# Optimization experiments

Measured on AMD Instinct MI355X. Metric: run time of the kernel, lower is better.

The kernel has to match this reference:

```python
import jax, jax.numpy as jnp
import numpy as np

B, N, F_IN = 4, 2048, 256
K, D = 4, 64
NEG_SLOPE = 0.2


def setup_inputs() -> dict:
    key = jax.random.key(0)
    k1, k2, k3, k4, k5 = jax.random.split(key, 5)
    x = jax.random.normal(k1, (B, N, F_IN), dtype=jnp.float32)
    adj = jax.random.randint(k2, (B, N, N), 0, 2, dtype=jnp.int32)
    # xavier_uniform-style params
    def xavier(k, shape):
        fan_in, fan_out = shape[-2], shape[-1]
        lim = np.sqrt(6.0 / (fan_in + fan_out))
        return jax.random.uniform(k, shape, jnp.float32, -lim, lim)
    W = xavier(k3, (K, F_IN, D))
    a_src = xavier(k4, (K, D, 1))
    a_dst = xavier(k5, (K, D, 1))
    return {"x": x, "adj": adj, "W": W, "a_src": a_src, "a_dst": a_dst}


def reference(x, adj, W, a_src, a_dst):
    # Wh: (B, K, N, D)
    Wh = jnp.einsum('bnf,kfd->bknd', x, W)
    e_src = jnp.einsum('bknd,kdo->bkno', Wh, a_src)  # (B,K,N,1)
    e_dst = jnp.einsum('bknd,kdo->bkno', Wh, a_dst)  # (B,K,N,1)
    e = e_src + jnp.swapaxes(e_dst, -2, -1)          # (B,K,N,N)
    e = jnp.where(e > 0, e, NEG_SLOPE * e)           # LeakyReLU(0.2)
    # adjacency mask with forced self-loops (adj + I > 0)
    eye = jnp.eye(e.shape[-1], dtype=bool)
    mask = (adj[:, None, :, :] > 0) | eye            # (B,1|K,N,N)
    e = jnp.where(mask, e, -jnp.inf)
    # numerically-stable softmax matching F_module_softmax
    x_max = jnp.max(e, axis=-1, keepdims=True)
    x_max = jnp.where(jnp.isinf(x_max), 0.0, x_max)
    exp_e = jnp.exp(e - x_max)
    exp_e = jnp.where(jnp.isinf(e), 0.0, exp_e)
    alpha = exp_e / (jnp.sum(exp_e, axis=-1, keepdims=True) + 1e-10)
    # dropout is identity in eval mode
    out = jnp.matmul(alpha, Wh)                      # (B,K,N,D)
    # concat heads: (B,N,K*D)
    Bn, Kn, Nn, Dn = out.shape
    return jnp.transpose(out, (0, 2, 1, 3)).reshape(Bn, Nn, Kn * Dn)
```

## Files before the change

### kernel.cpp

```cpp
#include <hip/hip_runtime.h>

#define NB 4
#define NN 2048
#define NF 256
#define NK 4
#define ND 64
#define NEG 0.2f
#define LOG2E 1.4426950408889634f

typedef _Float16 f16;
typedef _Float16 f16x4 __attribute__((ext_vector_type(4)));
typedef _Float16 f16x8 __attribute__((ext_vector_type(8)));
typedef float f32x4 __attribute__((ext_vector_type(4)));

__device__ __forceinline__ int sz2(int d) { return ((d >> 1) ^ (d >> 3)) & 3; }

__global__ __launch_bounds__(256) void k01(
    const float* __restrict__ x,
    const int*   __restrict__ adj,
    const float* __restrict__ Wm,
    const float* __restrict__ a_src,
    const float* __restrict__ a_dst,
    unsigned int* __restrict__ abit,
    f16* __restrict__ wht,
    float* __restrict__ sbuf,
    float* __restrict__ ebuf,
    float* __restrict__ fbuf)
{
    __shared__ f16 wt[64 * 256];

    const int bx  = blockIdx.x;
    const int tid = threadIdx.x;

    if (bx >= 256) {
        const int row = (bx - 256) * 4 + (tid >> 6);
        const int l   = tid & 63;
        const int i   = row & (NN - 1);
        const int* __restrict__ ar = adj + (size_t)row * NN;

        int v[32];
#pragma unroll
        for (int c = 0; c < 32; ++c) v[c] = ar[c * 64 + l];

        unsigned int kx = 0, ky = 0;
#pragma unroll
        for (int c = 0; c < 32; ++c) {
            unsigned long long m = __ballot(v[c] > 0);
            if (l == c) { kx = (unsigned int)m; ky = (unsigned int)(m >> 32); }
        }
        if (l == (i >> 6)) {
            unsigned int sb = 1u << (i & 31);
            if (((i >> 5) & 1) == 0) kx |= sb; else ky |= sb;
        }
        if (l < 32) {
            uint2 kk; kk.x = kx; kk.y = ky;
            *(uint2*)&abit[(size_t)row * 64 + l * 2] = kk;
        }
        return;
    }

    const int gx  = bx & 15;
    const int k   = (bx >> 4) & 3;
    const int b   = bx >> 6;
    const int wv  = tid >> 6;
    const int l   = tid & 63;
    const int q   = l >> 4;
    const int r16 = l & 15;

    for (int fc = 0; fc < 64; ++fc) {
        int f = fc * 4 + wv;
        int d = l;
        wt[d * 256 + (f ^ ((d & 7) << 3))] = (f16)Wm[(k * NF + f) * ND + d];
    }
    __syncthreads();

    const int ncol0 = gx * 128 + wv * 32;
    f32x4 acc[2][4];
#pragma unroll
    for (int nt = 0; nt < 2; ++nt)
#pragma unroll
        for (int dt = 0; dt < 4; ++dt)
            acc[nt][dt] = (f32x4){0.f, 0.f, 0.f, 0.f};

    for (int fs = 0; fs < 16; ++fs) {
        const int f0 = fs * 16 + q * 4;
        f16x4 af[4];
#pragma unroll
        for (int dt = 0; dt < 4; ++dt) {
            int d = dt * 16 + r16;
            af[dt] = *(const f16x4*)&wt[d * 256 + (f0 ^ ((d & 7) << 3))];
        }
#pragma unroll
        for (int nt = 0; nt < 2; ++nt) {
            int n = ncol0 + nt * 16 + r16;
            float4 xv = *(const float4*)&x[((size_t)(b * NN + n)) * NF + f0];
            f16x4 bf = {(f16)xv.x, (f16)xv.y, (f16)xv.z, (f16)xv.w};
#pragma unroll
            for (int dt = 0; dt < 4; ++dt)
                acc[nt][dt] = __builtin_amdgcn_mfma_f32_16x16x16f16(
                    af[dt], bf, acc[nt][dt], 0, 0, 0);
        }
    }

    float asv[4][4], adv[4][4];
#pragma unroll
    for (int dt = 0; dt < 4; ++dt)
#pragma unroll
        for (int rr = 0; rr < 4; ++rr) {
            int d = dt * 16 + q * 4 + rr;
            asv[dt][rr] = a_src[k * ND + d];
            adv[dt][rr] = a_dst[k * ND + d];
        }

    const int jt = gx * 4 + wv;
    f16* __restrict__ tile = wht + ((size_t)(b * NK + k) * 64 + jt) * 2048;
    const int qj = r16 >> 2, ee = r16 & 3;

#pragma unroll
    for (int nt = 0; nt < 2; ++nt) {
        int n = ncol0 + nt * 16 + r16;
        float sp = 0.f, tp = 0.f;
#pragma unroll
        for (int dt = 0; dt < 4; ++dt)
#pragma unroll
            for (int rr = 0; rr < 4; ++rr) {
                float v = acc[nt][dt][rr];
                int d = dt * 16 + q * 4 + rr;
                tile[d * 32 + ((qj ^ sz2(d)) << 3) + nt * 4 + ee] = (f16)v;
                sp += v * asv[dt][rr];
                tp += v * adv[dt][rr];
            }
        sp += __shfl_xor(sp, 16);
        sp += __shfl_xor(sp, 32);
        tp += __shfl_xor(tp, 16);
        tp += __shfl_xor(tp, 32);
        if (q == 0) {
            int idx = (b * NK + k) * NN + n;
            sbuf[idx] = sp;
            ebuf[idx] = __builtin_exp2f(tp * LOG2E);
            fbuf[idx] = __builtin_exp2f(0.2f * LOG2E * tp);
        }
    }
}

__global__ __launch_bounds__(512, 4) void k2_attn(
    const unsigned int* __restrict__ abit,
    const f16* __restrict__ wht,
    const float* __restrict__ sbuf,
    const float* __restrict__ ebuf,
    const float* __restrict__ fbuf,
    float* __restrict__ out)
{
    const int i0  = blockIdx.x * 64;
    const int k   = blockIdx.y;
    const int b   = blockIdx.z;
    const int tid = threadIdx.x;
    const int w   = tid >> 6;
    const int c   = w >> 2;
    const int rw  = w & 3;
    const int l   = tid & 63;
    const int q   = l >> 4;
    const int r16 = l & 15;
    const int iglob = i0 + rw * 16 + r16;

    __shared__ char pool[66048];
    float* el   = (float*)(pool + 49152);
    float* fl   = (float*)(pool + 57344);
    float* dden = (float*)(pool + 65536);

    const unsigned int* __restrict__ abrow =
        abit + (size_t)(b * NN + iglob) * 64 + c * 32;
    uint2 abx[16];
#pragma unroll
    for (int it = 0; it < 16; ++it) abx[it] = *(const uint2*)(abrow + it * 2);

    {
        const float* eb = ebuf + (b * NK + k) * NN;
        const float* fb = fbuf + (b * NK + k) * NN;
        *(float4*)&el[tid * 4] = *(const float4*)&eb[tid * 4];
        *(float4*)&fl[tid * 4] = *(const float4*)&fb[tid * 4];
    }

    const float s  = sbuf[(b * NK + k) * NN + iglob];
    const float Af = __builtin_exp2f(0.8f * LOG2E * fminf(s, 0.f));
    const float Bf = __builtin_exp2f(-0.8f * LOG2E * fmaxf(s, 0.f));
    const char* gtiles = (const char*)(wht + (size_t)(b * NK + k) * 64 * 2048);

    float denom = 0.f;
    f32x4 acc[4];
#pragma unroll
    for (int dt = 0; dt < 4; ++dt) acc[dt] = (f32x4){0.f, 0.f, 0.f, 0.f};

#define STAGE8(bb, it)                                                         \
    do {                                                                       \
        const char* gsrc = gtiles + (size_t)(c * 1024 + (it) * 64) * 128 +     \
                           (tid & 255) * 16;                                   \
        char* ldst = pool + c * 24576 + (bb) * 8192 + (w & 3) * 1024;          \
        __builtin_amdgcn_global_load_lds(                                      \
            (const __attribute__((address_space(1))) void*)gsrc,               \
            (__attribute__((address_space(3))) void*)ldst, 16, 0, 0);          \
        __builtin_amdgcn_global_load_lds(                                      \
            (const __attribute__((address_space(1))) void*)(gsrc + 4096),      \
            (__attribute__((address_space(3))) void*)(ldst + 4096), 16, 0, 0); \
    } while (0)

    STAGE8(0, 0);
    STAGE8(1, 1);

#pragma unroll
    for (int it = 0; it < 16; ++it) {
        if (it < 15)
            asm volatile("s_waitcnt vmcnt(2) lgkmcnt(0)" ::: "memory");
        else
            asm volatile("s_waitcnt vmcnt(0) lgkmcnt(0)" ::: "memory");
        __builtin_amdgcn_sched_barrier(0);
        __builtin_amdgcn_s_barrier();
        __builtin_amdgcn_sched_barrier(0);
        if (it < 14) STAGE8((it + 2) % 3, it + 2);

        const char* lb0 = pool + c * 24576 + (it % 3) * 8192;
        const uint2 ab = abx[it];
#pragma unroll
        for (int h = 0; h < 2; ++h) {
            const unsigned int bits = h ? ab.y : ab.x;
            const unsigned int bs = bits >> (q * 4);
            const int tb = c * 1024 + it * 64 + h * 32;
            float4 e0 = *(const float4*)&el[tb + q * 4];
            float4 e1 = *(const float4*)&el[tb + 16 + q * 4];
            float4 f0 = *(const float4*)&fl[tb + q * 4];
            float4 f1 = *(const float4*)&fl[tb + 16 + q * 4];
            float ea[4] = {e0.x, e0.y, e0.z, e0.w};
            float eb[4] = {e1.x, e1.y, e1.z, e1.w};
            float fa[4] = {f0.x, f0.y, f0.z, f0.w};
            float fb[4] = {f1.x, f1.y, f1.z, f1.w};
            float w0[4], w1[4];
#pragma unroll
            for (int e = 0; e < 4; ++e) {
                float wa = fmaxf(Af * ea[e], Bf * fa[e]);
                w0[e] = (bs & (1u << e)) ? wa : 0.f;
                float wb = fmaxf(Af * eb[e], Bf * fb[e]);
                w1[e] = (bs & (1u << (16 + e))) ? wb : 0.f;
            }
            denom += ((w0[0] + w0[1]) + (w0[2] + w0[3])) +
                     ((w1[0] + w1[1]) + (w1[2] + w1[3]));
            f16x8 pa = {(f16)w0[0], (f16)w0[1], (f16)w0[2], (f16)w0[3],
                        (f16)w1[0], (f16)w1[1], (f16)w1[2], (f16)w1[3]};
            const char* lb = lb0 + h * 4096;
#pragma unroll
            for (int dt = 0; dt < 4; ++dt) {
                int d = dt * 16 + r16;
                f16x8 v8 = *(const f16x8*)(lb + d * 64 + ((q ^ sz2(d)) << 4));
                acc[dt] = __builtin_amdgcn_mfma_f32_16x16x32_f16(
                    pa, v8, acc[dt], 0, 0, 0);
            }
        }
    }
#undef STAGE8

    denom += __shfl_xor(denom, 16);
    denom += __shfl_xor(denom, 32);

    __syncthreads();
    float* stash = (float*)pool;
    if (c == 1) {
#pragma unroll
        for (int dt = 0; dt < 4; ++dt)
            *(f32x4*)&stash[(rw * 4 + dt) * 256 + l * 4] = acc[dt];
    }
    if (l < 16) dden[c * 64 + rw * 16 + l] = denom;
    __syncthreads();

    if (c == 0) {
#pragma unroll
        for (int dt = 0; dt < 4; ++dt)
            acc[dt] += *(const f32x4*)&stash[(rw * 4 + dt) * 256 + l * 4];
#pragma unroll
        for (int rr = 0; rr < 4; ++rr) {
            int irow = q * 4 + rr;
            float dd = dden[rw * 16 + irow] + dden[64 + rw * 16 + irow];
            float inv = 1.f / (dd + 1e-10f);
#pragma unroll
            for (int dt = 0; dt < 4; ++dt)
                out[((size_t)(b * NN) + i0 + rw * 16 + irow) * (NK * ND) +
                    k * ND + dt * 16 + r16] = acc[dt][rr] * inv;
        }
    }
}

extern "C" void kernel_launch(void* const* d_in, const int* in_sizes, int n_in,
                              void* d_out, int out_size, void* d_ws, size_t ws_size,
                              hipStream_t stream) {
    const float* x     = (const float*)d_in[0];
    const int*   adj   = (const int*)d_in[1];
    const float* Wm    = (const float*)d_in[2];
    const float* a_src = (const float*)d_in[3];
    const float* a_dst = (const float*)d_in[4];
    float* out = (float*)d_out;

    char* ws = (char*)d_ws;
    f16*   wht  = (f16*)ws;
    float* sbuf = (float*)(ws + (4u << 20));
    float* ebuf = (float*)(ws + (4u << 20) + (128u << 10));
    float* fbuf = (float*)(ws + (4u << 20) + (256u << 10));
    unsigned int* abit = (unsigned int*)(ws + (4u << 20) + (384u << 10));

    k01<<<dim3(256 + NB * NN / 4), 256, 0, stream>>>(
        x, adj, Wm, a_src, a_dst, abit, wht, sbuf, ebuf, fbuf);
    k2_attn<<<dim3(NN / 64, NK, NB), 512, 0, stream>>>(
        abit, wht, sbuf, ebuf, fbuf, out);
}
```

Before: 47.76 us.

## Switch attention kernel to 32x32 MFMA tiles with 128-row blocks and 4-way j split

The attention kernel now processes 128 query rows per block with 1024 threads, splitting the neighbor dimension four ways across wave groups and using 32x32x16 MFMA instead of 16x16x32. The Wh staging layout written by the first kernel is changed to 64-column slabs with an 8-way XOR swizzle to match the new LDS read pattern. The cross-group reduction stashes three partial accumulators with a swizzle and sums them in group 0. The aim is more reuse of each staged Wh tile across more rows and fewer MFMA issues. In exchange it needs much more LDS (about 114KB), which limits occupancy, and a heavier final reduction.

```diff
diff --git a/kernel.cpp b/kernel.cpp
--- a/kernel.cpp
+++ b/kernel.cpp
@@ -12,8 +12,9 @@
 typedef _Float16 f16x4 __attribute__((ext_vector_type(4)));
 typedef _Float16 f16x8 __attribute__((ext_vector_type(8)));
 typedef float f32x4 __attribute__((ext_vector_type(4)));
-
-__device__ __forceinline__ int sz2(int d) { return ((d >> 1) ^ (d >> 3)) & 3; }
+typedef float f32x16 __attribute__((ext_vector_type(16)));
+
+__device__ __forceinline__ int gsz(int d) { return (d ^ (d >> 3)) & 7; }
 
 __global__ __launch_bounds__(256) void k01(
     const float* __restrict__ x,
@@ -112,13 +113,12 @@
             adv[dt][rr] = a_dst[k * ND + d];
         }
 
-    const int jt = gx * 4 + wv;
-    f16* __restrict__ tile = wht + ((size_t)(b * NK + k) * 64 + jt) * 2048;
-    const int qj = r16 >> 2, ee = r16 & 3;
+    const size_t obase = (size_t)(b * NK + k) * 131072;
 
 #pragma unroll
     for (int nt = 0; nt < 2; ++nt) {
-        int n = ncol0 + nt * 16 + r16;
+        int n  = ncol0 + nt * 16 + r16;
+        int s_ = n >> 6, g = (n >> 3) & 7, e = n & 7;
         float sp = 0.f, tp = 0.f;
 #pragma unroll
         for (int dt = 0; dt < 4; ++dt)
@@ -126,7 +126,7 @@
             for (int rr = 0; rr < 4; ++rr) {
                 float v = acc[nt][dt][rr];
                 int d = dt * 16 + q * 4 + rr;
-                tile[d * 32 + ((qj ^ sz2(d)) << 3) + nt * 4 + ee] = (f16)v;
+                wht[obase + s_ * 4096 + d * 64 + ((g ^ gsz(d)) << 3) + e] = (f16)v;
                 sp += v * asv[dt][rr];
                 tp += v * adv[dt][rr];
             }
@@ -143,7 +143,7 @@
     }
 }
 
-__global__ __launch_bounds__(512, 4) void k2_attn(
+__global__ __launch_bounds__(1024, 4) void k2_attn(
     const unsigned int* __restrict__ abit,
     const f16* __restrict__ wht,
     const float* __restrict__ sbuf,
@@ -151,7 +151,7 @@
     const float* __restrict__ fbuf,
     float* __restrict__ out)
 {
-    const int i0  = blockIdx.x * 64;
+    const int i0  = blockIdx.x * 128;
     const int k   = blockIdx.y;
     const int b   = blockIdx.z;
     const int tid = threadIdx.x;
@@ -159,43 +159,46 @@
     const int c   = w >> 2;
     const int rw  = w & 3;
     const int l   = tid & 63;
-    const int q   = l >> 4;
-    const int r16 = l & 15;
-    const int iglob = i0 + rw * 16 + r16;
-
-    __shared__ char pool[66048];
-    float* el   = (float*)(pool + 49152);
-    float* fl   = (float*)(pool + 57344);
-    float* dden = (float*)(pool + 65536);
+    const int r32 = l & 31;
+    const int hi  = l >> 5;
+    const int iglob = i0 + rw * 32 + r32;
+
+    __shared__ __attribute__((aligned(16))) char pool[116736];
+    float* el   = (float*)(pool + 98304);
+    float* fl   = (float*)(pool + 106496);
+    float* dden = (float*)(pool + 114688);
 
     const unsigned int* __restrict__ abrow =
-        abit + (size_t)(b * NN + iglob) * 64 + c * 32;
-    uint2 abx[16];
-#pragma unroll
-    for (int it = 0; it < 16; ++it) abx[it] = *(const uint2*)(abrow + it * 2);
+        abit + (size_t)(b * NN + iglob) * 64 + c * 16;
+    uint2 abx[8];
+#pragma unroll
+    for (int it = 0; it < 8; ++it) abx[it] = *(const uint2*)(abrow + it * 2);
 
     {
         const float* eb = ebuf + (b * NK + k) * NN;
         const float* fb = fbuf + (b * NK + k) * NN;
-        *(float4*)&el[tid * 4] = *(const float4*)&eb[tid * 4];
-        *(float4*)&fl[tid * 4] = *(const float4*)&fb[tid * 4];
+        int t5 = tid & 511;
+        if (tid < 512) *(float4*)&el[t5 * 4] = *(const float4*)&eb[t5 * 4];
+        else           *(float4*)&fl[t5 * 4] = *(const float4*)&fb[t5 * 4];
     }
 
     const float s  = sbuf[(b * NK + k) * NN + iglob];
     const float Af = __builtin_exp2f(0.8f * LOG2E * fminf(s, 0.f));
     const float Bf = __builtin_exp2f(-0.8f * LOG2E * fmaxf(s, 0.f));
-    const char* gtiles = (const char*)(wht + (size_t)(b * NK + k) * 64 * 2048);
+    const char* gtiles = (const char*)wht + (size_t)(b * NK + k) * 262144;
 
     float denom = 0.f;
-    f32x4 acc[4];
-#pragma unroll
-    for (int dt = 0; dt < 4; ++dt) acc[dt] = (f32x4){0.f, 0.f, 0.f, 0.f};
+    f32x16 acc[2];
+#pragma unroll
+    for (int dh = 0; dh < 2; ++dh)
+#pragma unroll
+        for (int z = 0; z < 16; ++z) acc[dh][z] = 0.f;
 
 #define STAGE8(bb, it)                                                         \
     do {                                                                       \
-        const char* gsrc = gtiles + (size_t)(c * 1024 + (it) * 64) * 128 +     \
+        const char* gsrc = gtiles + (size_t)(c * 8 + (it)) * 8192 +            \
                            (tid & 255) * 16;                                   \
-        char* ldst = pool + c * 24576 + (bb) * 8192 + (w & 3) * 1024;          \
+        char* ldst = pool + c * 24576 + (bb) * 8192 + (tid & 255) * 16;        \
         __builtin_amdgcn_global_load_lds(                                      \
             (const __attribute__((address_space(1))) void*)gsrc,               \
             (__attribute__((address_space(3))) void*)ldst, 16, 0, 0);          \
@@ -204,85 +207,104 @@
             (__attribute__((address_space(3))) void*)(ldst + 4096), 16, 0, 0); \
     } while (0)
 
+    __builtin_amdgcn_sched_barrier(0);
     STAGE8(0, 0);
     STAGE8(1, 1);
 
 #pragma unroll
-    for (int it = 0; it < 16; ++it) {
-        if (it < 15)
-            asm volatile("s_waitcnt vmcnt(2) lgkmcnt(0)" ::: "memory");
-        else
-            asm volatile("s_waitcnt vmcnt(0) lgkmcnt(0)" ::: "memory");
+    for (int it = 0; it < 8; ++it) {
+        if (it < 7) asm volatile("s_waitcnt vmcnt(2) lgkmcnt(0)" ::: "memory");
+        else        asm volatile("s_waitcnt vmcnt(0) lgkmcnt(0)" ::: "memory");
         __builtin_amdgcn_sched_barrier(0);
         __builtin_amdgcn_s_barrier();
         __builtin_amdgcn_sched_barrier(0);
-        if (it < 14) STAGE8((it + 2) % 3, it + 2);
-
-        const char* lb0 = pool + c * 24576 + (it % 3) * 8192;
+        if (it < 6) STAGE8((it + 2) % 3, it + 2);
+
+        const char* lb = pool + c * 24576 + (it % 3) * 8192;
         const uint2 ab = abx[it];
 #pragma unroll
-        for (int h = 0; h < 2; ++h) {
-            const unsigned int bits = h ? ab.y : ab.x;
-            const unsigned int bs = bits >> (q * 4);
-            const int tb = c * 1024 + it * 64 + h * 32;
-            float4 e0 = *(const float4*)&el[tb + q * 4];
-            float4 e1 = *(const float4*)&el[tb + 16 + q * 4];
-            float4 f0 = *(const float4*)&fl[tb + q * 4];
-            float4 f1 = *(const float4*)&fl[tb + 16 + q * 4];
-            float ea[4] = {e0.x, e0.y, e0.z, e0.w};
-            float eb[4] = {e1.x, e1.y, e1.z, e1.w};
-            float fa[4] = {f0.x, f0.y, f0.z, f0.w};
-            float fb[4] = {f1.x, f1.y, f1.z, f1.w};
-            float w0[4], w1[4];
-#pragma unroll
-            for (int e = 0; e < 4; ++e) {
-                float wa = fmaxf(Af * ea[e], Bf * fa[e]);
-                w0[e] = (bs & (1u << e)) ? wa : 0.f;
-                float wb = fmaxf(Af * eb[e], Bf * fb[e]);
-                w1[e] = (bs & (1u << (16 + e))) ? wb : 0.f;
-            }
-            denom += ((w0[0] + w0[1]) + (w0[2] + w0[3])) +
-                     ((w1[0] + w1[1]) + (w1[2] + w1[3]));
-            f16x8 pa = {(f16)w0[0], (f16)w0[1], (f16)w0[2], (f16)w0[3],
-                        (f16)w1[0], (f16)w1[1], (f16)w1[2], (f16)w1[3]};
-            const char* lb = lb0 + h * 4096;
-#pragma unroll
-            for (int dt = 0; dt < 4; ++dt) {
-                int d = dt * 16 + r16;
-                f16x8 v8 = *(const f16x8*)(lb + d * 64 + ((q ^ sz2(d)) << 4));
-                acc[dt] = __builtin_amdgcn_mfma_f32_16x16x32_f16(
-                    pa, v8, acc[dt], 0, 0, 0);
+        for (int jj = 0; jj < 4; ++jj) {
+            const int jts = (jj + c) & 3;
+            const unsigned int word  = (jts & 2) ? ab.y : ab.x;
+            const unsigned int mbyte = (word >> (((jts & 1) << 4) + (hi << 3))) & 0xffu;
+            const int jb = c * 512 + it * 64 + jts * 16 + hi * 8;
+            float4 e0 = *(const float4*)&el[jb];
+            float4 e1 = *(const float4*)&el[jb + 4];
+            float4 f0 = *(const float4*)&fl[jb];
+            float4 f1 = *(const float4*)&fl[jb + 4];
+            float ev[8] = {e0.x, e0.y, e0.z, e0.w, e1.x, e1.y, e1.z, e1.w};
+            float fv[8] = {f0.x, f0.y, f0.z, f0.w, f1.x, f1.y, f1.z, f1.w};
+            float wv[8];
+#pragma unroll
+            for (int e = 0; e < 8; ++e) {
+                float m = fmaxf(Af * ev[e], Bf * fv[e]);
+                wv[e] = (mbyte & (1u << e)) ? m : 0.f;
+            }
+            denom += ((wv[0] + wv[1]) + (wv[2] + wv[3])) +
+                     ((wv[4] + wv[5]) + (wv[6] + wv[7]));
+            f16x8 pa = {(f16)wv[0], (f16)wv[1], (f16)wv[2], (f16)wv[3],
+                        (f16)wv[4], (f16)wv[5], (f16)wv[6], (f16)wv[7]};
+#pragma unroll
+            for (int dh = 0; dh < 2; ++dh) {
+                const int d = dh * 32 + r32;
+                f16x8 v8 = *(const f16x8*)(lb + d * 128 +
+                               ((((jts << 1) | hi) ^ gsz(d)) << 4));
+                acc[dh] = __builtin_amdgcn_mfma_f32_32x32x16_f16(
+                    pa, v8, acc[dh], 0, 0, 0);
             }
         }
     }
 #undef STAGE8
 
-    denom += __shfl_xor(denom, 16);
     denom += __shfl_xor(denom, 32);
 
     __syncthreads();
     float* stash = (float*)pool;
-    if (c == 1) {
-#pragma unroll
-        for (int dt = 0; dt < 4; ++dt)
-            *(f32x4*)&stash[(rw * 4 + dt) * 256 + l * 4] = acc[dt];
-    }
-    if (l < 16) dden[c * 64 + rw * 16 + l] = denom;
+    if (c != 0) {
+        float* sb = stash + ((c - 1) * 4 + rw) * 2048 + l * 16;
+#pragma unroll
+        for (int dh = 0; dh < 2; ++dh)
+#pragma unroll
+            for (int sub = 0; sub < 4; ++sub) {
+                f32x4 v = {acc[dh][sub * 4], acc[dh][sub * 4 + 1],
+                           acc[dh][sub * 4 + 2], acc[dh][sub * 4 + 3]};
+                *(f32x4*)&sb[dh * 1024 + ((sub ^ (l & 3)) << 2)] = v;
+            }
+    }
+    if (l < 32) dden[c * 128 + rw * 32 + l] = denom;
     __syncthreads();
 
     if (c == 0) {
 #pragma unroll
-        for (int dt = 0; dt < 4; ++dt)
-            acc[dt] += *(const f32x4*)&stash[(rw * 4 + dt) * 256 + l * 4];
-#pragma unroll
-        for (int rr = 0; rr < 4; ++rr) {
-            int irow = q * 4 + rr;
-            float dd = dden[rw * 16 + irow] + dden[64 + rw * 16 + irow];
-            float inv = 1.f / (dd + 1e-10f);
-#pragma unroll
-            for (int dt = 0; dt < 4; ++dt)
-                out[((size_t)(b * NN) + i0 + rw * 16 + irow) * (NK * ND) +
-                    k * ND + dt * 16 + r16] = acc[dt][rr] * inv;
+        for (int cc = 0; cc < 3; ++cc) {
+            const float* sr = stash + (cc * 4 + rw) * 2048 + l * 16;
+#pragma unroll
+            for (int dh = 0; dh < 2; ++dh)
+#pragma unroll
+                for (int sub = 0; sub < 4; ++sub) {
+                    f32x4 v = *(const f32x4*)&sr[dh * 1024 + ((sub ^ (l & 3)) << 2)];
+#pragma unroll
+                    for (int m = 0; m < 4; ++m) acc[dh][sub * 4 + m] += v[m];
+                }
+        }
+        float* op = out + ((size_t)(b * NN) + i0 + rw * 32) * (NK * ND) + k * ND;
+#pragma unroll
+        for (int g4 = 0; g4 < 4; ++g4) {
+            f32x4 ds = {0.f, 0.f, 0.f, 0.f};
+#pragma unroll
+            for (int c4 = 0; c4 < 4; ++c4) {
+                f32x4 dv = *(const f32x4*)&dden[c4 * 128 + rw * 32 + g4 * 8 + hi * 4];
+#pragma unroll
+                for (int m = 0; m < 4; ++m) ds[m] += dv[m];
+            }
+#pragma unroll
+            for (int m = 0; m < 4; ++m) {
+                const int rr   = g4 * 4 + m;
+                const int irow = g4 * 8 + hi * 4 + m;
+                const float inv = 1.f / (ds[m] + 1e-10f);
+                op[(size_t)irow * (NK * ND) + r32]      = acc[0][rr] * inv;
+                op[(size_t)irow * (NK * ND) + 32 + r32] = acc[1][rr] * inv;
+            }
         }
     }
 }
@@ -306,6 +328,6 @@
 
     k01<<<dim3(256 + NB * NN / 4), 256, 0, stream>>>(
         x, adj, Wm, a_src, a_dst, abit, wht, sbuf, ebuf, fbuf);
-    k2_attn<<<dim3(NN / 64, NK, NB), 512, 0, stream>>>(
+    k2_attn<<<dim3(NN / 128, NK, NB), 1024, 0, stream>>>(
         abit, wht, sbuf, ebuf, fbuf, out);
 }
```

New measurement: 46.38 us. -2.9%, faster.
